# Performance work log

Measured on AMD Instinct MI355X. Metric: run time of the kernel, lower is better.

Reference implementation:

```python
import jax, jax.numpy as jnp
import numpy as np

B, S, D, H = 4, 1024, 1024, 16
DH = D // H  # per-head dim


def setup_inputs() -> dict:
    key = jax.random.key(0)
    ks = jax.random.split(key, 9)
    f = lambda k, sh: jax.random.normal(k, sh, dtype=jnp.float32)
    return {
        "query": f(ks[0], (B, S, D)),
        "key": f(ks[1], (B, S, D)),
        "value": f(ks[2], (B, S, D)),
        "mask": jax.random.randint(ks[3], (B, S), 0, 2).astype(jnp.int32),
        "pos_emb": f(ks[4], (H, S, DH)),
        "W_q": f(ks[5], (D, D)) * 0.02,
        "W_k": f(ks[6], (D, D)) * 0.02,
        "W_v": f(ks[7], (D, D)) * 0.02,
        "W_o": f(ks[8], (D, D)) * 0.02,
    }


def _shift(x):
    """Music-Transformer skew trick. x: [b,h,i,j] -> [b,h,i,j]."""
    b, h, i, j = x.shape
    x = jnp.concatenate([x, jnp.zeros((b, h, i, i), x.dtype)], axis=-1)  # [b,h,i,i+j]
    l = i + j - 1
    flat = x.reshape(b, h, i * (i + j))
    pad = (-flat.shape[-1]) % l
    flat = jnp.concatenate([flat, jnp.zeros((b, h, pad), flat.dtype)], axis=-1)
    return flat.reshape(b, h, -1, l)[:, :, :i, i - 1:]


def reference(query, key, value, mask, pos_emb, W_q, W_k, W_v, W_o):
    b, s, _ = query.shape
    # torch Linear(bias=False): y = x @ W.T ; then split heads -> [b,h,s,dh]
    proj = lambda x, W: (x @ W.T).reshape(b, s, H, DH).transpose(0, 2, 1, 3)
    q = proj(query, W_q)
    k = proj(key, W_k)
    v = proj(value, W_v)

    dots = jnp.einsum('bhid,bhjd->bhij', q, k) * (DH ** -0.5)
    pe = pos_emb[:, :s, :]  # [h,s,dh]
    # NOTE: original code scales positional scores by dim ** (+0.5)
    pos_dots = jnp.einsum('bhid,hjd->bhij', q, pe) * (DH ** 0.5)
    dots = dots + _shift(pos_dots)

    m = (mask[:, :, None] * mask[:, None, :])[:, None]  # [b,1,s,s]
    dots = jnp.where(m == 0, jnp.float32(-1e9), dots)

    attn = jax.nn.softmax(dots, axis=-1)  # dropout omitted (eval / p=0)
    x = jnp.einsum('bhij,bhjd->bhid', attn, v)
    x = x.transpose(0, 2, 1, 3).reshape(b, s, H * DH)
    return x @ W_o.T
```

## Files before the change

### kernel.cpp

```cpp
#include <hip/hip_runtime.h>
#include <math.h>

#define BB 4
#define SS 1024
#define DD 1024
#define HH 16
#define DHH 64

typedef _Float16 half8 __attribute__((ext_vector_type(8)));
typedef _Float16 half4v __attribute__((ext_vector_type(4)));
typedef float v4f __attribute__((ext_vector_type(4)));
typedef unsigned int u32;
typedef unsigned short u16;

__device__ __forceinline__ void gload_lds16(const void* g, void* l) {
    __builtin_amdgcn_global_load_lds(
        (const __attribute__((address_space(1))) u32*)(const u32*)g,
        (__attribute__((address_space(3))) u32*)(u32*)l, 16, 0, 0);
}

__global__ __launch_bounds__(256) void convert_kernel(
    const float* __restrict__ wq, const float* __restrict__ wk,
    const float* __restrict__ wv, const float* __restrict__ wo,
    const float* __restrict__ pe, _Float16* __restrict__ dst)
{
    const int i4 = blockIdx.x * 256 + threadIdx.x;
    const int region = i4 >> 18;
    const int local4 = i4 & 262143;
    const float* srcs[5] = {wq, wk, wv, wo, pe};
    const float scales[5] = {1.0f, 0.125f, 1.0f, 1.0f, 8.0f};
    const float sc = scales[region];
    float4 v = *(const float4*)(srcs[region] + (size_t)local4 * 4);
    half4v h = {(_Float16)(v.x * sc), (_Float16)(v.y * sc),
                (_Float16)(v.z * sc), (_Float16)(v.w * sc)};
    *(half4v*)(dst + ((size_t)region << 20) + (size_t)local4 * 4) = h;
}

__global__ __launch_bounds__(256) void gemm_proj(
    const float* __restrict__ Aq, const float* __restrict__ Ak,
    const float* __restrict__ Av,
    const _Float16* __restrict__ Wqf, const _Float16* __restrict__ Wkf,
    const _Float16* __restrict__ Wvf,
    _Float16* __restrict__ Cq, _Float16* __restrict__ Ck,
    _Float16* __restrict__ Cv)
{
    __shared__ _Float16 As[128 * 32];
    __shared__ _Float16 Bs[64 * 32];

    const int z = blockIdx.z;
    const float* A = z == 0 ? Aq : z == 1 ? Ak : Av;
    const _Float16* W = z == 0 ? Wqf : z == 1 ? Wkf : Wvf;
    _Float16* C = z == 0 ? Cq : z == 1 ? Ck : Cv;

    const int tid = threadIdx.x;
    const int w = tid >> 6, lane = tid & 63, lm = lane & 15, quad = lane >> 4;
    const int n0 = blockIdx.x * 64, m0 = blockIdx.y * 128;

    const int brow = tid >> 2, blc = (tid & 3) ^ (brow & 3);

    v4f zero4 = {0.f, 0.f, 0.f, 0.f};
    v4f acc[2][4];
#pragma unroll
    for (int mi = 0; mi < 2; mi++)
#pragma unroll
        for (int ni = 0; ni < 4; ni++) acc[mi][ni] = zero4;

    for (int k0 = 0; k0 < DD; k0 += 32) {
        __syncthreads();
        gload_lds16(W + (size_t)(n0 + brow) * DD + k0 + blc * 8, Bs + tid * 8);
#pragma unroll
        for (int u = 0; u < 4; u++) {
            int c4 = tid + 256 * u;
            int row = c4 >> 3, k4 = c4 & 7;
            float4 v = *(const float4*)(A + (size_t)(m0 + row) * DD + k0 + k4 * 4);
            half4v hv = {(_Float16)v.x, (_Float16)v.y, (_Float16)v.z, (_Float16)v.w};
            int c16 = k4 >> 1, hlf = k4 & 1;
            *(half4v*)(As + row * 32 + (((c16 ^ (row & 3)) << 3) + (hlf << 2))) = hv;
        }
        __syncthreads();

        half8 af[2], bf[4];
#pragma unroll
        for (int mi = 0; mi < 2; mi++) {
            int row = w * 32 + mi * 16 + lm;
            af[mi] = *(const half8*)(As + row * 32 + ((quad ^ (row & 3)) << 3));
        }
#pragma unroll
        for (int ni = 0; ni < 4; ni++) {
            int row = ni * 16 + lm;
            bf[ni] = *(const half8*)(Bs + row * 32 + ((quad ^ (row & 3)) << 3));
        }
#pragma unroll
        for (int mi = 0; mi < 2; mi++)
#pragma unroll
            for (int ni = 0; ni < 4; ni++)
                acc[mi][ni] = __builtin_amdgcn_mfma_f32_16x16x32_f16(
                    af[mi], bf[ni], acc[mi][ni], 0, 0, 0);
    }

    const int h = n0 >> 6;
#pragma unroll
    for (int mi = 0; mi < 2; mi++)
#pragma unroll
        for (int r = 0; r < 4; r++) {
            int m = m0 + w * 32 + mi * 16 + quad * 4 + r;
            int b = m >> 10, s = m & 1023;
            size_t base = ((size_t)(b * HH + h) * SS + s) * DHH;
#pragma unroll
            for (int ni = 0; ni < 4; ni++)
                C[base + ni * 16 + lm] = (_Float16)acc[mi][ni][r];
        }
}

__global__ __launch_bounds__(256) void gemm_out(
    const _Float16* __restrict__ A, const _Float16* __restrict__ W,
    float* __restrict__ C)
{
    __shared__ _Float16 As[128 * 32];
    __shared__ _Float16 Bs[64 * 32];

    const int tid = threadIdx.x;
    const int w = tid >> 6, lane = tid & 63, lm = lane & 15, quad = lane >> 4;
    const int n0 = blockIdx.x * 64, m0 = blockIdx.y * 128;
    const int brow = tid >> 2, blc = (tid & 3) ^ (brow & 3);

    v4f zero4 = {0.f, 0.f, 0.f, 0.f};
    v4f acc[2][4];
#pragma unroll
    for (int mi = 0; mi < 2; mi++)
#pragma unroll
        for (int ni = 0; ni < 4; ni++) acc[mi][ni] = zero4;

    for (int k0 = 0; k0 < DD; k0 += 32) {
        __syncthreads();
        gload_lds16(W + (size_t)(n0 + brow) * DD + k0 + blc * 8, Bs + tid * 8);
#pragma unroll
        for (int u = 0; u < 2; u++) {
            int p = tid + 256 * u;
            int row = p >> 2, lc = (p & 3) ^ (row & 3);
            gload_lds16(A + (size_t)(m0 + row) * DD + k0 + lc * 8, As + p * 8);
        }
        __syncthreads();

        half8 af[2], bf[4];
#pragma unroll
        for (int mi = 0; mi < 2; mi++) {
            int row = w * 32 + mi * 16 + lm;
            af[mi] = *(const half8*)(As + row * 32 + ((quad ^ (row & 3)) << 3));
        }
#pragma unroll
        for (int ni = 0; ni < 4; ni++) {
            int row = ni * 16 + lm;
            bf[ni] = *(const half8*)(Bs + row * 32 + ((quad ^ (row & 3)) << 3));
        }
#pragma unroll
        for (int mi = 0; mi < 2; mi++)
#pragma unroll
            for (int ni = 0; ni < 4; ni++)
                acc[mi][ni] = __builtin_amdgcn_mfma_f32_16x16x32_f16(
                    af[mi], bf[ni], acc[mi][ni], 0, 0, 0);
    }

#pragma unroll
    for (int mi = 0; mi < 2; mi++)
#pragma unroll
        for (int r = 0; r < 4; r++) {
            size_t base = (size_t)(m0 + w * 32 + mi * 16 + quad * 4 + r) * DD
                        + n0 + lm;
#pragma unroll
            for (int ni = 0; ni < 4; ni++)
                C[base + ni * 16] = acc[mi][ni][r];
        }
}

__global__ __launch_bounds__(256) void attn_mfma(
    const _Float16* __restrict__ Qg, const _Float16* __restrict__ Kg,
    const _Float16* __restrict__ Vg, const int* __restrict__ mask,
    const _Float16* __restrict__ peg, _Float16* __restrict__ Og)
{
    __shared__ _Float16 Ks[64 * 72];
    __shared__ _Float16 Vt[64 * 72];
    __shared__ _Float16 PEb[128 * 72];
    __shared__ _Float16 Pb[4][16 * 72];

    const int tid = threadIdx.x;
    const int w = tid >> 6, lane = tid & 63;
    const int lm = lane & 15, quad = lane >> 4;
    const int it = blockIdx.x, i0 = it * 64;
    const int bh = blockIdx.y, b = bh >> 4, h = bh & 15;

    const _Float16* Qb = Qg + (size_t)bh * SS * DHH;
    const _Float16* Kb = Kg + (size_t)bh * SS * DHH;
    const _Float16* Vb = Vg + (size_t)bh * SS * DHH;
    const _Float16* peh = peg + (size_t)h * SS * DHH;

    float mi_f[4];
#pragma unroll
    for (int r = 0; r < 4; r++)
        mi_f[r] = (float)mask[b * SS + i0 + w * 16 + quad * 4 + r];

    half8 qf[2];
#pragma unroll
    for (int kc = 0; kc < 2; kc++)
        qf[kc] = *(const half8*)(Qb + (size_t)(i0 + w * 16 + lm) * DHH
                                 + kc * 32 + quad * 8);

    v4f zero4 = {0.f, 0.f, 0.f, 0.f};
    float m_run[4], l_run[4];
    v4f oacc[4];
#pragma unroll
    for (int r = 0; r < 4; r++) { m_run[r] = -1e30f; l_run[r] = 0.f; }
#pragma unroll
    for (int nb = 0; nb < 4; nb++) oacc[nb] = zero4;

    for (int jt = 0; jt < SS / 64; jt++) {
        const int j0 = jt * 64;
        const bool do_pe = (jt <= it);
        __syncthreads();

#pragma unroll
        for (int u = 0; u < 2; u++) {
            int c = tid + 256 * u;
            int row = c >> 3, k8 = c & 7;
            half8 v = *(const half8*)(Kb + (size_t)(j0 + row) * DHH + k8 * 8);
            *(half8*)(Ks + row * 72 + k8 * 8) = v;
        }
#pragma unroll
        for (int u = 0; u < 2; u++) {
            int c = tid + 256 * u;
            int row = c >> 3, k8 = c & 7;
            half8 v = *(const half8*)(Vb + (size_t)(j0 + row) * DHH + k8 * 8);
            int jsw = row ^ (k8 << 3);
#pragma unroll
            for (int e = 0; e < 8; e++) Vt[(k8 * 8 + e) * 72 + jsw] = v[e];
        }
        if (do_pe) {
            const int g0 = SS - 1 + j0 - i0 - 63;
#pragma unroll
            for (int u = 0; u < 4; u++) {
                int c = tid + 256 * u;
                int o = c >> 3, k8 = c & 7;
                int g = g0 + o;
                half8 v = {0, 0, 0, 0, 0, 0, 0, 0};
                if (g < SS) v = *(const half8*)(peh + (size_t)g * DHH + k8 * 8);
                *(half8*)(PEb + o * 72 + k8 * 8) = v;
            }
        }
        float mj_f[4];
#pragma unroll
        for (int nb = 0; nb < 4; nb++)
            mj_f[nb] = (float)mask[b * SS + j0 + nb * 16 + lm];
        __syncthreads();

        v4f sacc[4];
#pragma unroll
        for (int nb = 0; nb < 4; nb++) sacc[nb] = zero4;
        __builtin_amdgcn_s_setprio(1);
#pragma unroll
        for (int nb = 0; nb < 4; nb++)
#pragma unroll
            for (int kc = 0; kc < 2; kc++) {
                half8 kf = *(const half8*)(Ks + (nb * 16 + lm) * 72 + kc * 32 + quad * 8);
                sacc[nb] = __builtin_amdgcn_mfma_f32_16x16x32_f16(qf[kc], kf, sacc[nb], 0, 0, 0);
            }
        __builtin_amdgcn_s_setprio(0);

        if (do_pe) {
            v4f racc[5];
#pragma unroll
            for (int e = 0; e < 5; e++) racc[e] = zero4;
            __builtin_amdgcn_s_setprio(1);
#pragma unroll
            for (int e = 0; e < 5; e++) {
                int row = (e + 3 - w) * 16 + lm;
#pragma unroll
                for (int kc = 0; kc < 2; kc++) {
                    half8 pf = *(const half8*)(PEb + row * 72 + kc * 32 + quad * 8);
                    racc[e] = __builtin_amdgcn_mfma_f32_16x16x32_f16(qf[kc], pf, racc[e], 0, 0, 0);
                }
            }
            __builtin_amdgcn_s_setprio(0);
#pragma unroll
            for (int nb = 0; nb < 4; nb++)
#pragma unroll
                for (int r = 0; r < 4; r++) {
                    int qr = quad * 4 + r;
                    float vsrc = (((lm + qr + 1) & 15) <= qr)
                               ? racc[nb][r] : racc[nb + 1][r];
                    int src = (lane & 48) | ((lm - qr - 1) & 15);
                    sacc[nb][r] += __shfl(vsrc, src);
                }
        }

        float p[4][4];
        float alpha[4];
#pragma unroll
        for (int i = 0; i < 4; i++) {
            float mi = mi_f[i];
            float rmax = -1e30f;
#pragma unroll
            for (int j = 0; j < 4; j++) {
                float s = sacc[j][i];
                if (mi * mj_f[j] == 0.f) s = -1e9f;
                sacc[j][i] = s;
                rmax = fmaxf(rmax, s);
            }
#pragma unroll
            for (int off = 1; off < 16; off <<= 1)
                rmax = fmaxf(rmax, __shfl_xor(rmax, off));
            float mnew = fmaxf(m_run[i], rmax);
            alpha[i] = __expf(m_run[i] - mnew);
            m_run[i] = mnew;
            float rsum = 0.f;
#pragma unroll
            for (int j = 0; j < 4; j++) {
                p[j][i] = __expf(sacc[j][i] - mnew);
                rsum += p[j][i];
            }
#pragma unroll
            for (int off = 1; off < 16; off <<= 1)
                rsum += __shfl_xor(rsum, off);
            l_run[i] = l_run[i] * alpha[i] + rsum;
        }

        _Float16* Pw = &Pb[w][0];
#pragma unroll
        for (int nb = 0; nb < 4; nb++)
#pragma unroll
            for (int r = 0; r < 4; r++)
                Pw[(quad * 4 + r) * 72 + nb * 16 + lm] = (_Float16)p[nb][r];
#pragma unroll
        for (int nb = 0; nb < 4; nb++)
#pragma unroll
            for (int r = 0; r < 4; r++) oacc[nb][r] *= alpha[r];
        __syncthreads();

        __builtin_amdgcn_s_setprio(1);
#pragma unroll
        for (int kc = 0; kc < 2; kc++) {
            half8 pfrag = *(const half8*)(Pw + lm * 72 + kc * 32 + quad * 8);
#pragma unroll
            for (int nb = 0; nb < 4; nb++) {
                int d = nb * 16 + lm;
                int col = (kc * 32 + quad * 8) ^ (((d >> 3) & 7) << 3);
                half8 vfrag = *(const half8*)(Vt + d * 72 + col);
                oacc[nb] = __builtin_amdgcn_mfma_f32_16x16x32_f16(pfrag, vfrag, oacc[nb], 0, 0, 0);
            }
        }
        __builtin_amdgcn_s_setprio(0);
    }

#pragma unroll
    for (int r = 0; r < 4; r++) {
        float inv = 1.f / l_run[r];
        int s = i0 + w * 16 + quad * 4 + r;
#pragma unroll
        for (int nb = 0; nb < 4; nb++)
            Og[((size_t)b * SS + s) * DD + h * DHH + nb * 16 + lm] =
                (_Float16)(oacc[nb][r] * inv);
    }
}

extern "C" void kernel_launch(void* const* d_in, const int* in_sizes, int n_in,
                              void* d_out, int out_size, void* d_ws, size_t ws_size,
                              hipStream_t stream)
{
    const float* query = (const float*)d_in[0];
    const float* key   = (const float*)d_in[1];
    const float* value = (const float*)d_in[2];
    const int*   mask  = (const int*)d_in[3];
    const float* pe    = (const float*)d_in[4];
    const float* Wq    = (const float*)d_in[5];
    const float* Wk    = (const float*)d_in[6];
    const float* Wv    = (const float*)d_in[7];
    const float* Wo    = (const float*)d_in[8];
    float* out = (float*)d_out;

    _Float16* ws16 = (_Float16*)d_ws;
    const size_t MEG = 1048576;
    _Float16* wqf = ws16;
    _Float16* wkf = ws16 + 1 * MEG;
    _Float16* wvf = ws16 + 2 * MEG;
    _Float16* wof = ws16 + 3 * MEG;
    _Float16* pef = ws16 + 4 * MEG;
    _Float16* qp  = ws16 + 5 * MEG;
    _Float16* kp  = ws16 + 9 * MEG;
    _Float16* vp  = ws16 + 13 * MEG;
    _Float16* ao  = ws16 + 17 * MEG;

    convert_kernel<<<5120, 256, 0, stream>>>(Wq, Wk, Wv, Wo, pe, ws16);

    gemm_proj<<<dim3(DD / 64, (BB * SS) / 128, 3), 256, 0, stream>>>(
        query, key, value, wqf, wkf, wvf, qp, kp, vp);

    attn_mfma<<<dim3(SS / 64, BB * HH), 256, 0, stream>>>(qp, kp, vp, mask, pef, ao);

    gemm_out<<<dim3(DD / 64, (BB * SS) / 128), 256, 0, stream>>>(ao, wof, out);
}
```

Baseline: 313.8 us.

## Prefetch next K/V/PE tiles into registers and drop redundant barrier

```diff
diff --git a/kernel.cpp b/kernel.cpp
--- a/kernel.cpp
+++ b/kernel.cpp
@@ -205,6 +205,8 @@
         qf[kc] = *(const half8*)(Qb + (size_t)(i0 + w * 16 + lm) * DHH
                                  + kc * 32 + quad * 8);
 
+    const int srow = tid >> 3, sk8 = tid & 7;
+
     v4f zero4 = {0.f, 0.f, 0.f, 0.f};
     float m_run[4], l_run[4];
     v4f oacc[4];
@@ -213,6 +215,25 @@
 #pragma unroll
     for (int nb = 0; nb < 4; nb++) oacc[nb] = zero4;
 
+    half8 kreg[2], vreg[2], pereg[4];
+#pragma unroll
+    for (int u = 0; u < 2; u++) {
+        int row = srow + 32 * u;
+        kreg[u] = *(const half8*)(Kb + (size_t)row * DHH + sk8 * 8);
+        vreg[u] = *(const half8*)(Vb + (size_t)row * DHH + sk8 * 8);
+    }
+    {
+        const int g0 = SS - 1 - i0 - 63;
+#pragma unroll
+        for (int u = 0; u < 4; u++) {
+            int o = srow + 32 * u;
+            int g = g0 + o;
+            half8 v = {0, 0, 0, 0, 0, 0, 0, 0};
+            if (g < SS) v = *(const half8*)(peh + (size_t)g * DHH + sk8 * 8);
+            pereg[u] = v;
+        }
+    }
+
     for (int jt = 0; jt < SS / 64; jt++) {
         const int j0 = jt * 64;
         const bool do_pe = (jt <= it);
@@ -220,30 +241,21 @@
 
 #pragma unroll
         for (int u = 0; u < 2; u++) {
-            int c = tid + 256 * u;
-            int row = c >> 3, k8 = c & 7;
-            half8 v = *(const half8*)(Kb + (size_t)(j0 + row) * DHH + k8 * 8);
-            *(half8*)(Ks + row * 72 + k8 * 8) = v;
+            int row = srow + 32 * u;
+            *(half8*)(Ks + row * 72 + sk8 * 8) = kreg[u];
         }
 #pragma unroll
         for (int u = 0; u < 2; u++) {
-            int c = tid + 256 * u;
-            int row = c >> 3, k8 = c & 7;
-            half8 v = *(const half8*)(Vb + (size_t)(j0 + row) * DHH + k8 * 8);
-            int jsw = row ^ (k8 << 3);
-#pragma unroll
-            for (int e = 0; e < 8; e++) Vt[(k8 * 8 + e) * 72 + jsw] = v[e];
+            int row = srow + 32 * u;
+            int jsw = row ^ (sk8 << 3);
+#pragma unroll
+            for (int e = 0; e < 8; e++) Vt[(sk8 * 8 + e) * 72 + jsw] = vreg[u][e];
         }
         if (do_pe) {
-            const int g0 = SS - 1 + j0 - i0 - 63;
 #pragma unroll
             for (int u = 0; u < 4; u++) {
-                int c = tid + 256 * u;
-                int o = c >> 3, k8 = c & 7;
-                int g = g0 + o;
-                half8 v = {0, 0, 0, 0, 0, 0, 0, 0};
-                if (g < SS) v = *(const half8*)(peh + (size_t)g * DHH + k8 * 8);
-                *(half8*)(PEb + o * 72 + k8 * 8) = v;
+                int o = srow + 32 * u;
+                *(half8*)(PEb + o * 72 + sk8 * 8) = pereg[u];
             }
         }
         float mj_f[4];
@@ -251,6 +263,27 @@
         for (int nb = 0; nb < 4; nb++)
             mj_f[nb] = (float)mask[b * SS + j0 + nb * 16 + lm];
         __syncthreads();
+
+        if (jt + 1 < SS / 64) {
+            const int j0n = j0 + 64;
+#pragma unroll
+            for (int u = 0; u < 2; u++) {
+                int row = srow + 32 * u;
+                kreg[u] = *(const half8*)(Kb + (size_t)(j0n + row) * DHH + sk8 * 8);
+                vreg[u] = *(const half8*)(Vb + (size_t)(j0n + row) * DHH + sk8 * 8);
+            }
+            if (jt + 1 <= it) {
+                const int g0n = SS - 1 + j0n - i0 - 63;
+#pragma unroll
+                for (int u = 0; u < 4; u++) {
+                    int o = srow + 32 * u;
+                    int g = g0n + o;
+                    half8 v = {0, 0, 0, 0, 0, 0, 0, 0};
+                    if (g < SS) v = *(const half8*)(peh + (size_t)g * DHH + sk8 * 8);
+                    pereg[u] = v;
+                }
+            }
+        }
 
         v4f sacc[4];
 #pragma unroll
@@ -333,7 +366,6 @@
         for (int nb = 0; nb < 4; nb++)
 #pragma unroll
             for (int r = 0; r < 4; r++) oacc[nb][r] *= alpha[r];
-        __syncthreads();
 
         __builtin_amdgcn_s_setprio(1);
 #pragma unroll
```

Measured after the change: 306.6 us. 1.02x faster.
